# Kernel tuning notes

Hardware: AMD Instinct MI355X
Metric: run time of the kernel (lower is better)

Reference implementation:

```python
import jax, jax.numpy as jnp
import numpy as np

H = 64
VOCAB = 64
READ_FREQ = 16


def setup_inputs() -> dict:
    key = jax.random.key(0)
    ks = jax.random.split(key, 16)
    B, L, M = 512, 2048, 256
    seq = jax.random.randint(ks[0], (B, L), 0, VOCAB)
    memory = jax.random.normal(ks[1], (B, M, H), dtype=jnp.float32)
    s = 0.1
    return {
        "seq": seq,
        "memory": memory,
        "embed_w": jax.random.normal(ks[2], (VOCAB, H), jnp.float32) * s,
        "gru_w_ih": jax.random.normal(ks[3], (3 * H, 2 * H), jnp.float32) * s,
        "gru_w_hh": jax.random.normal(ks[4], (3 * H, H), jnp.float32) * s,
        "gru_b_ih": jax.random.normal(ks[5], (3 * H,), jnp.float32) * s,
        "gru_b_hh": jax.random.normal(ks[6], (3 * H,), jnp.float32) * s,
        "key_w": jax.random.normal(ks[7], (H, H), jnp.float32) * s,
        "key_b": jax.random.normal(ks[8], (H,), jnp.float32) * s,
        "val_w": jax.random.normal(ks[9], (H, H), jnp.float32) * s,
        "val_b": jax.random.normal(ks[10], (H,), jnp.float32) * s,
        "query_w": jax.random.normal(ks[11], (H, H), jnp.float32) * s,
        "query_b": jax.random.normal(ks[12], (H,), jnp.float32) * s,
        "head_w": jax.random.normal(ks[13], (VOCAB, H), jnp.float32) * s,
        "head_b": jax.random.normal(ks[14], (VOCAB,), jnp.float32) * s,
    }


def _forward(seq, memory, embed_w, gru_w_ih, gru_w_hh, gru_b_ih, gru_b_hh,
             key_w, key_b, val_w, val_b, query_w, query_b, head_w, head_b):
    B, L = seq.shape
    scale = 1.0 / (H ** 0.5)
    # memory is fixed: precompute keys/values once (B, M, H)
    k = jnp.einsum("bmh,kh->bmk", memory, key_w) + key_b
    v = jnp.einsum("bmh,kh->bmk", memory, val_w) + val_b
    # embed all tokens up front: (B, L, H) -> chunks (C, F, B, H)
    emb = embed_w[seq]
    C = L // READ_FREQ
    emb_chunks = emb.reshape(B, C, READ_FREQ, H).transpose(1, 2, 0, 3)

    def gru_step(carry, x_t):
        h, retrieved = carry
        inp = jnp.concatenate([x_t, retrieved], axis=-1)  # (B, 2H)
        gi = inp @ gru_w_ih.T + gru_b_ih                   # (B, 3H)
        gh = h @ gru_w_hh.T + gru_b_hh                     # (B, 3H)
        i_r, i_z, i_n = jnp.split(gi, 3, axis=-1)
        h_r, h_z, h_n = jnp.split(gh, 3, axis=-1)
        r = jax.nn.sigmoid(i_r + h_r)
        z = jax.nn.sigmoid(i_z + h_z)
        n = jnp.tanh(i_n + r * h_n)
        h_new = (1.0 - z) * n + z * h
        return (h_new, retrieved), None

    def chunk_step(h, chunk_emb):  # chunk_emb: (READ_FREQ, B, H)
        q = h @ query_w.T + query_b                        # (B, H)
        scores = jnp.einsum("bh,bmh->bm", q, k) * scale
        w = jax.nn.softmax(scores, axis=-1)
        retrieved = jnp.einsum("bm,bmh->bh", w, v)
        (h, _), _ = jax.lax.scan(gru_step, (h, retrieved), chunk_emb)
        return h, None

    h0 = jnp.zeros((B, H), dtype=memory.dtype)
    h, _ = jax.lax.scan(chunk_step, h0, emb_chunks)
    return h @ head_w.T + head_b                            # (B, VOCAB)


def reference(seq, memory, embed_w, gru_w_ih, gru_w_hh, gru_b_ih, gru_b_hh,
              key_w, key_b, val_w, val_b, query_w, query_b, head_w, head_b):
    return _forward(seq, memory, embed_w, gru_w_ih, gru_w_hh, gru_b_ih, gru_b_hh,
                    key_w, key_b, val_w, val_b, query_w, query_b, head_w, head_b)
```

## Files before the change

### kernel.cpp

```cpp
#include <hip/hip_runtime.h>
#include <hip/hip_fp16.h>


#define B_ 512
#define L_ 2048
#define M_ 256
#define H_ 64
#define C_ 128
#define F_ 16

typedef float v2f __attribute__((ext_vector_type(2)));
typedef _Float16 h2v __attribute__((ext_vector_type(2)));

#if __has_builtin(__builtin_amdgcn_fdot2)
__device__ __forceinline__ float FDOT2(h2v a, h2v b, float c) {
    return __builtin_amdgcn_fdot2(a, b, c, false);
}
#else
__device__ __forceinline__ float FDOT2(h2v a, h2v b, float c) {
    return c + (float)a[0]*(float)b[0] + (float)a[1]*(float)b[1];
}
#endif

__device__ __forceinline__ h2v bch(unsigned u) { return __builtin_bit_cast(h2v, u); }
__device__ __forceinline__ unsigned rl_u(unsigned v, int lane) {
    return (unsigned)__builtin_amdgcn_readlane((int)v, lane);
}
__device__ __forceinline__ float rl(float v, int lane) {
    return __int_as_float(__builtin_amdgcn_readlane(__float_as_int(v), lane));
}
__device__ __forceinline__ unsigned pkrtz(float a, float b) {
    auto r = __builtin_amdgcn_cvt_pkrtz(a, b);
    return __builtin_bit_cast(unsigned, r);
}
__device__ __forceinline__ float dot4(float4 a, float4 b) {
    return a.x*b.x + a.y*b.y + a.z*b.z + a.w*b.w;
}
__device__ __forceinline__ float fast_rcp(float x) { return __builtin_amdgcn_rcpf(x); }
__device__ __forceinline__ float sigm(float x) { return fast_rcp(1.f + __expf(-x)); }
__device__ __forceinline__ float tanh_f(float x) {
    float e2 = __expf(-2.f * fabsf(x));
    return copysignf((1.f - e2) * fast_rcp(1.f + e2), x);
}
__device__ __forceinline__ unsigned h2rn(float a, float b) {
    __half2 h = __floats2half2_rn(a, b);
    return __builtin_bit_cast(unsigned, h);
}

#define WS_KT    0u
#define WS_V     16777216u
#define WS_G     33554432u
#define WS_WPHH  33603584u
#define WS_WR    33628160u
#define WS_QP    33652736u
#define WS_KWP   33660928u
#define WS_VWP   33677312u

#define S_KT   0u
#define S_V    32768u
#define S_QP   66560u
#define S_P    74752u
#define SMEM_BYTES 75264u

__global__ void pack_weights(const float* __restrict__ w_ih,
                             const float* __restrict__ w_hh,
                             const float* __restrict__ qw,
                             const float* __restrict__ kw,
                             const float* __restrict__ vw,
                             unsigned* __restrict__ WPhh2,
                             unsigned* __restrict__ WR2p,
                             unsigned* __restrict__ QP2,
                             float4* __restrict__ KWP,
                             float4* __restrict__ VWP)
{
    int idx = blockIdx.x * 256 + threadIdx.x;
    if (idx < 6144) {
        int j = idx & 63, t = idx >> 6, g = t % 3, k2 = t / 3;
        const float* s = w_hh + (g*64 + j)*64 + 2*k2;
        WPhh2[idx] = h2rn(s[0], s[1]);
    } else if (idx < 12288) {
        int i = idx - 6144;
        int j = i & 63, t = i >> 6, g = t % 3, k2 = t / 3;
        const float* s = w_ih + (g*64 + j)*128 + 64 + 2*k2;
        WR2p[i] = h2rn(s[0], s[1]);
    } else if (idx < 14336) {
        int i = idx - 12288;
        int j = i & 63, k2 = i >> 6;
        const float* s = qw + j*64 + 2*k2;
        QP2[i] = h2rn(s[0], s[1]);
    } else if (idx < 15360) {
        int i = idx - 14336;
        int j = i & 63, k4 = i >> 6;
        const float* s = kw + j*64 + 4*k4;
        KWP[i] = make_float4(s[0], s[1], s[2], s[3]);
    } else if (idx < 16384) {
        int i = idx - 15360;
        int j = i & 63, k4 = i >> 6;
        const float* s = vw + j*64 + 4*k4;
        VWP[i] = make_float4(s[0], s[1], s[2], s[3]);
    }
}

__global__ __launch_bounds__(64) void build_G(const float* __restrict__ embed_w,
                                              const float* __restrict__ w_ih,
                                              const float* __restrict__ b_ih,
                                              float* __restrict__ G)
{
    int v = blockIdx.x, j = threadIdx.x;
    __shared__ float e_s[64];
    e_s[j] = embed_w[v*64 + j];
    __syncthreads();
    float a0 = b_ih[j], a1 = b_ih[64 + j], a2 = b_ih[128 + j];
    for (int k = 0; k < 64; ++k) {
        float e = e_s[k];
        a0 += e * w_ih[j*128 + k];
        a1 += e * w_ih[(64 + j)*128 + k];
        a2 += e * w_ih[(128 + j)*128 + k];
    }
    G[v*192 + j]       = a0;
    G[v*192 + 64 + j]  = a1;
    G[v*192 + 128 + j] = a2;
}

__global__ __launch_bounds__(256) void compute_kv(const float* __restrict__ memory,
                                                  const float* __restrict__ key_b,
                                                  const float* __restrict__ val_b,
                                                  const float4* __restrict__ KWP,
                                                  const float4* __restrict__ VWP,
                                                  unsigned* __restrict__ kT2,
                                                  unsigned* __restrict__ vT2)
{
    int wid = threadIdx.x >> 6;
    int o   = threadIdx.x & 63;
    int row = blockIdx.x * 4 + wid;
    int b = row >> 8, m = row & 255;
    __shared__ __align__(16) float mem_s[4][64];
    __shared__ float avs[4][64];
    mem_s[wid][o] = memory[(size_t)row * 64 + o];
    __syncthreads();
    float ak = key_b[o], av = val_b[o];
    const float4* m4 = (const float4*)mem_s[wid];
#pragma unroll
    for (int k4 = 0; k4 < 16; ++k4) {
        float4 mm = m4[k4];
        ak += dot4(mm, KWP[k4*64 + o]);
        av += dot4(mm, VWP[k4*64 + o]);
    }
    float nb = __shfl_xor(ak, 1);
    if ((o & 1) == 0)
        kT2[((size_t)b*32 + (o >> 1))*256 + m] = h2rn(ak, nb);
    avs[wid][o] = av;
    __syncthreads();
    if ((wid & 1) == 0) {
        vT2[((size_t)b*64 + o)*128 + (m >> 1)] = h2rn(avs[wid][o], avs[wid+1][o]);
    }
}

#define GRU_STEP(cg0, cg1, cg2) do {                                        \
    float gr = (cg0) + RrB, gz = (cg1) + RzB, gn = bhn;                     \
    _Pragma("unroll")                                                       \
    for (int kp = 0; kp < 32; ++kp) {                                       \
        h2v hhp = bch(rl_u(hpu, 2*kp));                                     \
        gr = FDOT2(hhp, wr2[kp], gr);                                       \
        gz = FDOT2(hhp, wz2[kp], gz);                                       \
        gn = FDOT2(hhp, wn2[kp], gn);                                       \
    }                                                                       \
    float r_ = sigm(gr);                                                    \
    float z_ = sigm(gz);                                                    \
    float n_ = tanh_f(((cg2) + Rn) + r_ * gn);                              \
    h = fmaf(z_, h - n_, n_);                                               \
    float hx_ = __shfl_xor(h, 1);                                           \
    hpu = pkrtz(h, hx_);                                                    \
} while (0)

__global__ __launch_bounds__(64, 1) void recurrent_main(
    const int*   __restrict__ seq,
    const float* __restrict__ b_hh,
    const float* __restrict__ query_b,
    const float* __restrict__ head_w,
    const float* __restrict__ head_b,
    const unsigned* __restrict__ kT2g,
    const unsigned* __restrict__ vT2g,
    const float* __restrict__ G,
    const unsigned* __restrict__ WPhh2,
    const unsigned* __restrict__ WR2p,
    const unsigned* __restrict__ QP2g,
    float* __restrict__ out)
{
    const int b = blockIdx.x;
    const int j = threadIdx.x;

    extern __shared__ __align__(16) char smem[];
    const uint4* kT2_lds = (const uint4*)(smem + S_KT);
    const unsigned* qp2  = (const unsigned*)(smem + S_QP);

    {
        const uint4* kTg = (const uint4*)(kT2g + (size_t)b * 8192);
        uint4* kTls = (uint4*)(smem + S_KT);
#pragma unroll
        for (int i = 0; i < 32; ++i) kTls[i*64 + j] = kTg[i*64 + j];
        const uint4* vg4 = (const uint4*)(vT2g + (size_t)b * 8192);
        uint4* vls4 = (uint4*)(smem + S_V);
#pragma unroll
        for (int i = 0; i < 32; ++i) {
            int t = i*64 + j;
            vls4[(t >> 5)*33 + (t & 31)] = vg4[t];
        }
        const uint4* qpg = (const uint4*)QP2g;
        uint4* qls = (uint4*)(smem + S_QP);
#pragma unroll
        for (int i = 0; i < 8; ++i) qls[i*64 + j] = qpg[i*64 + j];
    }

    h2v wr2[32], wz2[32], wn2[32];
#pragma unroll
    for (int k2 = 0; k2 < 32; ++k2) {
        wr2[k2] = bch(WPhh2[(k2*3 + 0)*64 + j]);
        wz2[k2] = bch(WPhh2[(k2*3 + 1)*64 + j]);
        wn2[k2] = bch(WPhh2[(k2*3 + 2)*64 + j]);
    }
    h2v rr2[32], rz2[32], rn2[32];
#pragma unroll
    for (int k2 = 0; k2 < 32; ++k2) {
        rr2[k2] = bch(WR2p[(k2*3 + 0)*64 + j]);
        rz2[k2] = bch(WR2p[(k2*3 + 1)*64 + j]);
        rn2[k2] = bch(WR2p[(k2*3 + 2)*64 + j]);
    }

    float h = 0.f;
    unsigned hpu = 0u;
    const float bhr = b_hh[j], bhz = b_hh[64 + j], bhn = b_hh[128 + j];
    const float qb  = query_b[j];

    const int* seqb = seq + (size_t)b * L_;
    const uint4* vrow = (const uint4*)(smem + S_V) + j*33;
    const uint4* p4   = (const uint4*)(smem + S_P);
    __builtin_amdgcn_wave_barrier();

    for (int c = 0; c < C_; ++c) {
        const int c16 = c * F_;

        const int4 pA = *(const int4*)(seqb + c16);
        const int4 pB = *(const int4*)(seqb + c16 + 4);
        const int4 pC = *(const int4*)(seqb + c16 + 8);
        const int4 pD = *(const int4*)(seqb + c16 + 12);

        float q = qb;
#pragma unroll 8
        for (int k2 = 0; k2 < 32; ++k2) {
            h2v pp = bch(qp2[k2*64 + j]);
            h2v hh = bch(rl_u(hpu, 2*k2));
            q = FDOT2(hh, pp, q);
        }

        float qx = __shfl_xor(q, 1);
        unsigned qpu = pkrtz(q, qx);
        float s0 = 0.f, s1 = 0.f, s2 = 0.f, s3 = 0.f;
#pragma unroll 8
        for (int t = 0; t < 32; ++t) {
            h2v qq = bch(rl_u(qpu, 2*t));
            uint4 kk = kT2_lds[t*64 + j];
            s0 = FDOT2(bch(kk.x), qq, s0);
            s1 = FDOT2(bch(kk.y), qq, s1);
            s2 = FDOT2(bch(kk.z), qq, s2);
            s3 = FDOT2(bch(kk.w), qq, s3);
        }
        const float scale = 0.125f;
        float4 p;
        p.x = __expf(s0*scale); p.y = __expf(s1*scale);
        p.z = __expf(s2*scale); p.w = __expf(s3*scale);
        float sum = (p.x + p.y) + (p.z + p.w);
#pragma unroll
        for (int o = 32; o > 0; o >>= 1) sum += __shfl_xor(sum, o);
        float inv = fast_rcp(sum);
        *(uint2*)(smem + S_P + (size_t)j*8) =
            make_uint2(pkrtz(p.x, p.y), pkrtz(p.z, p.w));
        __builtin_amdgcn_wave_barrier();

        float r0 = 0.f, r1 = 0.f, r2 = 0.f, r3 = 0.f;
#pragma unroll 8
        for (int qd = 0; qd < 32; ++qd) {
            uint4 vv = vrow[qd];
            uint4 pp = p4[qd];
            r0 = FDOT2(bch(pp.x), bch(vv.x), r0);
            r1 = FDOT2(bch(pp.y), bch(vv.y), r1);
            r2 = FDOT2(bch(pp.z), bch(vv.z), r2);
            r3 = FDOT2(bch(pp.w), bch(vv.w), r3);
        }
        float ret = ((r0 + r1) + (r2 + r3)) * inv;

        float rx = __shfl_xor(ret, 1);
        unsigned rpu = pkrtz(ret, rx);
        float Rr = 0.f, Rz = 0.f, Rn = 0.f;
#pragma unroll
        for (int k2 = 0; k2 < 32; ++k2) {
            h2v rr = bch(rl_u(rpu, 2*k2));
            Rr = FDOT2(rr, rr2[k2], Rr);
            Rz = FDOT2(rr, rz2[k2], Rz);
            Rn = FDOT2(rr, rn2[k2], Rn);
        }
        const float RrB = Rr + bhr, RzB = Rz + bhz;

#pragma unroll 1
        for (int g = 0; g < 4; ++g) {
            const bool gb1 = (g & 1), gb2 = (g & 2);
            int4 tlo, thi, tg;
            tlo.x = gb1 ? pB.x : pA.x; tlo.y = gb1 ? pB.y : pA.y;
            tlo.z = gb1 ? pB.z : pA.z; tlo.w = gb1 ? pB.w : pA.w;
            thi.x = gb1 ? pD.x : pC.x; thi.y = gb1 ? pD.y : pC.y;
            thi.z = gb1 ? pD.z : pC.z; thi.w = gb1 ? pD.w : pC.w;
            tg.x = gb2 ? thi.x : tlo.x; tg.y = gb2 ? thi.y : tlo.y;
            tg.z = gb2 ? thi.z : tlo.z; tg.w = gb2 ? thi.w : tlo.w;
            const float* GA = G + tg.x*192;
            const float* GB = G + tg.y*192;
            const float* GC = G + tg.z*192;
            const float* GD = G + tg.w*192;
            float gA0 = GA[j], gA1 = GA[64+j], gA2 = GA[128+j];
            float gB0 = GB[j], gB1 = GB[64+j], gB2 = GB[128+j];
            float gC0 = GC[j], gC1 = GC[64+j], gC2 = GC[128+j];
            float gD0 = GD[j], gD1 = GD[64+j], gD2 = GD[128+j];

            GRU_STEP(gA0, gA1, gA2);
            GRU_STEP(gB0, gB1, gB2);
            GRU_STEP(gC0, gC1, gC2);
            GRU_STEP(gD0, gD1, gD2);
        }
    }

    float o = head_b[j];
#pragma unroll
    for (int k4 = 0; k4 < 16; ++k4) {
        float h0 = rl(h, 4*k4+0), h1 = rl(h, 4*k4+1);
        float h2 = rl(h, 4*k4+2), h3 = rl(h, 4*k4+3);
        const float* hw = head_w + j*64 + 4*k4;
        o += h0*hw[0] + h1*hw[1] + h2*hw[2] + h3*hw[3];
    }
    out[(size_t)b*64 + j] = o;
}

extern "C" void kernel_launch(void* const* d_in, const int* in_sizes, int n_in,
                              void* d_out, int out_size, void* d_ws, size_t ws_size,
                              hipStream_t stream) {
    const int*   seq      = (const int*)  d_in[0];
    const float* memory   = (const float*)d_in[1];
    const float* embed_w  = (const float*)d_in[2];
    const float* w_ih     = (const float*)d_in[3];
    const float* w_hh     = (const float*)d_in[4];
    const float* b_ih     = (const float*)d_in[5];
    const float* b_hh     = (const float*)d_in[6];
    const float* key_w    = (const float*)d_in[7];
    const float* key_b    = (const float*)d_in[8];
    const float* val_w    = (const float*)d_in[9];
    const float* val_b    = (const float*)d_in[10];
    const float* query_w  = (const float*)d_in[11];
    const float* query_b  = (const float*)d_in[12];
    const float* head_w   = (const float*)d_in[13];
    const float* head_b   = (const float*)d_in[14];

    char* ws = (char*)d_ws;
    unsigned* kT2  = (unsigned*)(ws + WS_KT);
    unsigned* vT2  = (unsigned*)(ws + WS_V);
    float*    G    = (float*)   (ws + WS_G);
    unsigned* WPhh2 = (unsigned*)(ws + WS_WPHH);
    unsigned* WR2p  = (unsigned*)(ws + WS_WR);
    unsigned* QP2   = (unsigned*)(ws + WS_QP);
    float4*   KWP   = (float4*)  (ws + WS_KWP);
    float4*   VWP   = (float4*)  (ws + WS_VWP);

    (void)hipFuncSetAttribute((const void*)recurrent_main,
                              hipFuncAttributeMaxDynamicSharedMemorySize,
                              (int)SMEM_BYTES);

    pack_weights<<<64, 256, 0, stream>>>(w_ih, w_hh, query_w, key_w, val_w,
                                         WPhh2, WR2p, QP2, KWP, VWP);
    build_G<<<64, 64, 0, stream>>>(embed_w, w_ih, b_ih, G);
    compute_kv<<<(B_*M_)/4, 256, 0, stream>>>(memory, key_b, val_b, KWP, VWP, kT2, vT2);
    recurrent_main<<<B_, 64, SMEM_BYTES, stream>>>(seq, b_hh, query_b, head_w, head_b,
                                                   kT2, vT2, G, WPhh2, WR2p, QP2,
                                                   (float*)d_out);
}
```

Measured before the change: 1.382 ms.

## Fold query projection into attention keys to drop per-chunk query matmul

Precomputes the product of the key and query weights so attention scores are computed directly from h against transformed keys plus a per-memory-slot bias. This removes the 64x64 query projection, its shuffle and packing from every chunk of the serial recurrence, and frees the LDS that held query weights. It adds two small setup kernels and extra work in compute_kv, and changes the fp16 rounding path of the scores. It also reorders the GRU gate additions so the per-token input contribution is added after the dot product, shortening the dependency chain.

New measurement: 1.323 ms. -4.2%, faster.

```diff
diff --git a/kernel.cpp b/kernel.cpp
--- a/kernel.cpp
+++ b/kernel.cpp
@@ -55,22 +55,22 @@
 #define WS_QP    33652736u
 #define WS_KWP   33660928u
 #define WS_VWP   33677312u
+#define WS_KQF   33693696u
+#define WS_BQ    33710080u
+#define WS_KQV   33710336u
+#define WS_C0    33710592u
+#define WS_CB    33710848u
 
 #define S_KT   0u
 #define S_V    32768u
-#define S_QP   66560u
-#define S_P    74752u
-#define SMEM_BYTES 75264u
+#define S_P    66560u
+#define SMEM_BYTES 67072u
 
 __global__ void pack_weights(const float* __restrict__ w_ih,
                              const float* __restrict__ w_hh,
-                             const float* __restrict__ qw,
-                             const float* __restrict__ kw,
                              const float* __restrict__ vw,
                              unsigned* __restrict__ WPhh2,
                              unsigned* __restrict__ WR2p,
-                             unsigned* __restrict__ QP2,
-                             float4* __restrict__ KWP,
                              float4* __restrict__ VWP)
 {
     int idx = blockIdx.x * 256 + threadIdx.x;
@@ -83,21 +83,57 @@
         int j = i & 63, t = i >> 6, g = t % 3, k2 = t / 3;
         const float* s = w_ih + (g*64 + j)*128 + 64 + 2*k2;
         WR2p[i] = h2rn(s[0], s[1]);
-    } else if (idx < 14336) {
+    } else if (idx < 13312) {
         int i = idx - 12288;
-        int j = i & 63, k2 = i >> 6;
-        const float* s = qw + j*64 + 2*k2;
-        QP2[i] = h2rn(s[0], s[1]);
-    } else if (idx < 15360) {
-        int i = idx - 14336;
-        int j = i & 63, k4 = i >> 6;
-        const float* s = kw + j*64 + 4*k4;
-        KWP[i] = make_float4(s[0], s[1], s[2], s[3]);
-    } else if (idx < 16384) {
-        int i = idx - 15360;
         int j = i & 63, k4 = i >> 6;
         const float* s = vw + j*64 + 4*k4;
         VWP[i] = make_float4(s[0], s[1], s[2], s[3]);
+    }
+}
+
+__global__ __launch_bounds__(64) void fold_kq(const float* __restrict__ kw,
+                                              const float* __restrict__ qw,
+                                              const float* __restrict__ kb,
+                                              const float* __restrict__ qb,
+                                              float* __restrict__ KQf,
+                                              float* __restrict__ bqv,
+                                              float* __restrict__ kqv,
+                                              float* __restrict__ c0p)
+{
+    int d = blockIdx.x, j = threadIdx.x;
+    __shared__ float kcol[64], kbs[64], qbs[64];
+    kcol[j] = kw[j*64 + d];
+    kbs[j]  = kb[j];
+    qbs[j]  = qb[j];
+    __syncthreads();
+    float acc = 0.f, accq = 0.f;
+    for (int t = 0; t < 64; ++t) {
+        float kc = kcol[t];
+        acc  += kc * qw[t*64 + j];
+        accq += kc * qbs[t];
+    }
+    KQf[d*64 + j] = acc;
+    if (j == 0) kqv[d] = accq;
+    if (d == 0) {
+        float vb = 0.f;
+        for (int t = 0; t < 64; ++t) vb += kbs[t] * qw[t*64 + j];
+        bqv[j] = vb;
+        if (j == 0) {
+            float c0 = 0.f;
+            for (int t = 0; t < 64; ++t) c0 += kbs[t] * qbs[t];
+            *c0p = c0;
+        }
+    }
+}
+
+__global__ __launch_bounds__(256) void pack_kq(const float* __restrict__ KQf,
+                                               float4* __restrict__ KQP)
+{
+    int i = blockIdx.x * 256 + threadIdx.x;
+    if (i < 1024) {
+        int o = i & 63, k4 = i >> 6;
+        KQP[i] = make_float4(KQf[(4*k4+0)*64 + o], KQf[(4*k4+1)*64 + o],
+                             KQf[(4*k4+2)*64 + o], KQf[(4*k4+3)*64 + o]);
     }
 }
 
@@ -123,12 +159,15 @@
 }
 
 __global__ __launch_bounds__(256) void compute_kv(const float* __restrict__ memory,
-                                                  const float* __restrict__ key_b,
+                                                  const float* __restrict__ bqv,
                                                   const float* __restrict__ val_b,
-                                                  const float4* __restrict__ KWP,
+                                                  const float4* __restrict__ KQP,
                                                   const float4* __restrict__ VWP,
+                                                  const float* __restrict__ kqv,
+                                                  const float* __restrict__ c0p,
                                                   unsigned* __restrict__ kT2,
-                                                  unsigned* __restrict__ vT2)
+                                                  unsigned* __restrict__ vT2,
+                                                  float* __restrict__ cB)
 {
     int wid = threadIdx.x >> 6;
     int o   = threadIdx.x & 63;
@@ -138,18 +177,21 @@
     __shared__ float avs[4][64];
     mem_s[wid][o] = memory[(size_t)row * 64 + o];
     __syncthreads();
-    float ak = key_b[o], av = val_b[o];
-    const float4* m4 = (const float4*)mem_s[wid];
+    float ak = bqv[o], av = val_b[o], ac = *c0p;
+    const float4* m4  = (const float4*)mem_s[wid];
+    const float4* kq4 = (const float4*)kqv;
 #pragma unroll
     for (int k4 = 0; k4 < 16; ++k4) {
         float4 mm = m4[k4];
-        ak += dot4(mm, KWP[k4*64 + o]);
+        ak += dot4(mm, KQP[k4*64 + o]);
         av += dot4(mm, VWP[k4*64 + o]);
+        ac += dot4(mm, kq4[k4]);
     }
     float nb = __shfl_xor(ak, 1);
     if ((o & 1) == 0)
         kT2[((size_t)b*32 + (o >> 1))*256 + m] = h2rn(ak, nb);
     avs[wid][o] = av;
+    if (o == 0) cB[row] = ac;
     __syncthreads();
     if ((wid & 1) == 0) {
         vT2[((size_t)b*64 + o)*128 + (m >> 1)] = h2rn(avs[wid][o], avs[wid+1][o]);
@@ -157,7 +199,7 @@
 }
 
 #define GRU_STEP(cg0, cg1, cg2) do {                                        \
-    float gr = (cg0) + RrB, gz = (cg1) + RzB, gn = bhn;                     \
+    float gr = RrB, gz = RzB, gn = bhn;                                     \
     _Pragma("unroll")                                                       \
     for (int kp = 0; kp < 32; ++kp) {                                       \
         h2v hhp = bch(rl_u(hpu, 2*kp));                                     \
@@ -165,8 +207,8 @@
         gz = FDOT2(hhp, wz2[kp], gz);                                       \
         gn = FDOT2(hhp, wn2[kp], gn);                                       \
     }                                                                       \
-    float r_ = sigm(gr);                                                    \
-    float z_ = sigm(gz);                                                    \
+    float r_ = sigm(gr + (cg0));                                            \
+    float z_ = sigm(gz + (cg1));                                            \
     float n_ = tanh_f(((cg2) + Rn) + r_ * gn);                              \
     h = fmaf(z_, h - n_, n_);                                               \
     float hx_ = __shfl_xor(h, 1);                                           \
@@ -176,7 +218,6 @@
 __global__ __launch_bounds__(64, 1) void recurrent_main(
     const int*   __restrict__ seq,
     const float* __restrict__ b_hh,
-    const float* __restrict__ query_b,
     const float* __restrict__ head_w,
     const float* __restrict__ head_b,
     const unsigned* __restrict__ kT2g,
@@ -184,7 +225,7 @@
     const float* __restrict__ G,
     const unsigned* __restrict__ WPhh2,
     const unsigned* __restrict__ WR2p,
-    const unsigned* __restrict__ QP2g,
+    const float* __restrict__ cB,
     float* __restrict__ out)
 {
     const int b = blockIdx.x;
@@ -192,7 +233,6 @@
 
     extern __shared__ __align__(16) char smem[];
     const uint4* kT2_lds = (const uint4*)(smem + S_KT);
-    const unsigned* qp2  = (const unsigned*)(smem + S_QP);
 
     {
         const uint4* kTg = (const uint4*)(kT2g + (size_t)b * 8192);
@@ -206,10 +246,6 @@
             int t = i*64 + j;
             vls4[(t >> 5)*33 + (t & 31)] = vg4[t];
         }
-        const uint4* qpg = (const uint4*)QP2g;
-        uint4* qls = (uint4*)(smem + S_QP);
-#pragma unroll
-        for (int i = 0; i < 8; ++i) qls[i*64 + j] = qpg[i*64 + j];
     }
 
     h2v wr2[32], wz2[32], wn2[32];
@@ -230,7 +266,7 @@
     float h = 0.f;
     unsigned hpu = 0u;
     const float bhr = b_hh[j], bhz = b_hh[64 + j], bhn = b_hh[128 + j];
-    const float qb  = query_b[j];
+    const float4 cc = *(const float4*)(cB + (size_t)b*256 + 4*j);
 
     const int* seqb = seq + (size_t)b * L_;
     const uint4* vrow = (const uint4*)(smem + S_V) + j*33;
@@ -245,20 +281,10 @@
         const int4 pC = *(const int4*)(seqb + c16 + 8);
         const int4 pD = *(const int4*)(seqb + c16 + 12);
 
-        float q = qb;
-#pragma unroll 8
-        for (int k2 = 0; k2 < 32; ++k2) {
-            h2v pp = bch(qp2[k2*64 + j]);
-            h2v hh = bch(rl_u(hpu, 2*k2));
-            q = FDOT2(hh, pp, q);
-        }
-
-        float qx = __shfl_xor(q, 1);
-        unsigned qpu = pkrtz(q, qx);
-        float s0 = 0.f, s1 = 0.f, s2 = 0.f, s3 = 0.f;
+        float s0 = cc.x, s1 = cc.y, s2 = cc.z, s3 = cc.w;
 #pragma unroll 8
         for (int t = 0; t < 32; ++t) {
-            h2v qq = bch(rl_u(qpu, 2*t));
+            h2v qq = bch(rl_u(hpu, 2*t));
             uint4 kk = kT2_lds[t*64 + j];
             s0 = FDOT2(bch(kk.x), qq, s0);
             s1 = FDOT2(bch(kk.y), qq, s1);
@@ -363,19 +389,26 @@
     float*    G    = (float*)   (ws + WS_G);
     unsigned* WPhh2 = (unsigned*)(ws + WS_WPHH);
     unsigned* WR2p  = (unsigned*)(ws + WS_WR);
-    unsigned* QP2   = (unsigned*)(ws + WS_QP);
-    float4*   KWP   = (float4*)  (ws + WS_KWP);
+    float4*   KQP   = (float4*)  (ws + WS_KWP);
     float4*   VWP   = (float4*)  (ws + WS_VWP);
+    float*    KQf   = (float*)   (ws + WS_KQF);
+    float*    bqv   = (float*)   (ws + WS_BQ);
+    float*    kqv   = (float*)   (ws + WS_KQV);
+    float*    c0p   = (float*)   (ws + WS_C0);
+    float*    cB    = (float*)   (ws + WS_CB);
 
     (void)hipFuncSetAttribute((const void*)recurrent_main,
                               hipFuncAttributeMaxDynamicSharedMemorySize,
                               (int)SMEM_BYTES);
 
-    pack_weights<<<64, 256, 0, stream>>>(w_ih, w_hh, query_w, key_w, val_w,
-                                         WPhh2, WR2p, QP2, KWP, VWP);
+    pack_weights<<<64, 256, 0, stream>>>(w_ih, w_hh, val_w, WPhh2, WR2p, VWP);
+    fold_kq<<<64, 64, 0, stream>>>(key_w, query_w, key_b, query_b,
+                                   KQf, bqv, kqv, c0p);
+    pack_kq<<<4, 256, 0, stream>>>(KQf, KQP);
     build_G<<<64, 64, 0, stream>>>(embed_w, w_ih, b_ih, G);
-    compute_kv<<<(B_*M_)/4, 256, 0, stream>>>(memory, key_b, val_b, KWP, VWP, kT2, vT2);
-    recurrent_main<<<B_, 64, SMEM_BYTES, stream>>>(seq, b_hh, query_b, head_w, head_b,
-                                                   kT2, vT2, G, WPhh2, WR2p, QP2,
+    compute_kv<<<(B_*M_)/4, 256, 0, stream>>>(memory, bqv, val_b, KQP, VWP,
+                                              kqv, c0p, kT2, vT2, cB);
+    recurrent_main<<<B_, 64, SMEM_BYTES, stream>>>(seq, b_hh, head_w, head_b,
+                                                   kT2, vT2, G, WPhh2, WR2p, cB,
                                                    (float*)d_out);
 }
```
